# Kernel tuning notes

Hardware: AMD Instinct MI355X
Metric: run time of the kernel (lower is better)

The kernel has to match this reference:

```python
import jax, jax.numpy as jnp
import numpy as np

N_ATOMS = 100000
N_EDGES = 6400000
CUTOFF = 12.0
CUTOFF_SR = 2.0
CUTOFF_SQ = CUTOFF * CUTOFF
KEHALF = 7.199822675975274  # ASE kehalf, unit factors = 1


def poly6_switch(d, cutoff):
    # Poly6 smooth switch-off: 1 at d=0, 0 at d>=cutoff
    x = d / cutoff
    sw = 1.0 - 10.0 * x**3 + 15.0 * x**4 - 6.0 * x**5
    return jnp.where(d < cutoff, sw, jnp.zeros_like(sw))


def setup_inputs() -> dict:
    key = jax.random.key(0)
    k1, k2, k3, k4, k5 = jax.random.split(key, 5)
    atomic_charges = jax.random.normal(k1, (N_ATOMS,), dtype=jnp.float32) * 0.3
    atomic_dipoles = jax.random.normal(k2, (N_ATOMS,), dtype=jnp.float32) * 0.1
    # distances in (0.5, 13.5): some pairs inside short-range, some beyond cutoff
    distances = jax.random.uniform(k3, (N_EDGES,), dtype=jnp.float32) * 13.0 + 0.5
    idx_i = jax.random.randint(k4, (N_EDGES,), 0, N_ATOMS, dtype=jnp.int32)
    idx_j = jax.random.randint(k5, (N_EDGES,), 0, N_ATOMS, dtype=jnp.int32)
    return {
        "atomic_charges": atomic_charges,
        "atomic_dipoles": atomic_dipoles,
        "distances": distances,
        "idx_i": idx_i,
        "idx_j": idx_j,
    }


def reference(atomic_charges, atomic_dipoles, distances, idx_i, idx_j):
    # gather per-edge charges / dipoles
    qi = atomic_charges[idx_i]
    qj = atomic_charges[idx_j]
    di = atomic_dipoles[idx_i]
    dj = atomic_dipoles[idx_j]

    d = distances
    d_sh = jnp.sqrt(d * d + 1.0)  # shielded distance

    sw_off = poly6_switch(d, CUTOFF_SR)
    sw_on = 1.0 - sw_off

    # split_distance=True branch (cutoff != cutoff_short_range):
    # shifted-force Coulomb (charge-charge, ~1/d)
    E_ord_q = 1.0 / d + d / CUTOFF_SQ - 2.0 / CUTOFF
    E_sh_q = 1.0 / d_sh + d_sh / CUTOFF_SQ - 2.0 / CUTOFF
    E_q = KEHALF * qi * qj * (sw_off * E_sh_q + sw_on * E_ord_q)

    # dipole-dipole term (~1/d^3), same shielded/ordinary blending
    E_ord_d = 1.0 / d**3
    E_sh_d = 1.0 / d_sh**3
    E_d = KEHALF * di * dj * (sw_off * E_sh_d + sw_on * E_ord_d)

    E = E_q + E_d
    E = jnp.where(d <= CUTOFF, E, jnp.zeros_like(E))

    # scatter-sum per-edge energies to atoms
    return jax.ops.segment_sum(E, idx_i, num_segments=N_ATOMS)
```

## Files before the change

kernel.cpp:

```cpp
#include <hip/hip_runtime.h>
#include <hip/hip_bf16.h>
#include <hip/hip_fp16.h>

#define CUTOFF_C    12.0f
#define CUTOFF_SR_C 2.0f
#define CUTOFF_SQ_C 144.0f
#define KEHALF_C    7.199822675975274f

#define BLK1   1024

#define CH_DUO   17408
#define LUT_DUO  1024
#define CH_SOLO  33792
#define LUT_SOLO 2048

#define CH_REC   20000

__device__ __forceinline__ float edge_energy(float d, float qi, float qj,
                                             float di, float dj) {
    float inv_d   = __frcp_rn(d);
    float dsh     = __fsqrt_rn(fmaf(d, d, 1.0f));
    float inv_dsh = __frcp_rn(dsh);
    float x  = d * (1.0f / CUTOFF_SR_C);
    float x3 = x * x * x;
    float sw = fmaf(x3, fmaf(x, fmaf(x, -6.0f, 15.0f), -10.0f), 1.0f);
    float sw_off = (d < CUTOFF_SR_C) ? sw : 0.0f;
    float Eoq = inv_d   + fmaf(d,   (1.0f / CUTOFF_SQ_C), -(2.0f / CUTOFF_C));
    float Esq = inv_dsh + fmaf(dsh, (1.0f / CUTOFF_SQ_C), -(2.0f / CUTOFF_C));
    float Eq  = (KEHALF_C * qi * qj) * fmaf(sw_off, Esq - Eoq, Eoq);
    float Eod = inv_d * inv_d * inv_d;
    float Esd = inv_dsh * inv_dsh * inv_dsh;
    float Ed  = (KEHALF_C * di * dj) * fmaf(sw_off, Esd - Eod, Eod);
    return Eq + Ed;
}

__device__ __forceinline__ float2 fg_exact(float d) {
    float inv_d   = 1.0f / d;
    float dsh     = sqrtf(fmaf(d, d, 1.0f));
    float inv_dsh = 1.0f / dsh;
    float x  = d * (1.0f / CUTOFF_SR_C);
    float x3 = x * x * x;
    float sw = fmaf(x3, fmaf(x, fmaf(x, -6.0f, 15.0f), -10.0f), 1.0f);
    float sw_off = (d < CUTOFF_SR_C) ? sw : 0.0f;
    float Foq = inv_d   + fmaf(d,   (1.0f / CUTOFF_SQ_C), -(2.0f / CUTOFF_C));
    float Fsq = inv_dsh + fmaf(dsh, (1.0f / CUTOFF_SQ_C), -(2.0f / CUTOFF_C));
    float F   = fmaf(sw_off, Fsq - Foq, Foq);
    float God = inv_d * inv_d * inv_d;
    float Gsd = inv_dsh * inv_dsh * inv_dsh;
    float G   = fmaf(sw_off, Gsd - God, God);
    return make_float2(KEHALF_C * F, KEHALF_C * G);
}

__device__ __forceinline__ __half2 vw_make_exact(float d, __half2 hqdj) {
    float2 qdj = __half22float2(hqdj);
    float2 fg  = fg_exact(d);
    return __floats2half2_rn(qdj.x * fg.x, qdj.y * fg.y);
}

__device__ __forceinline__ unsigned h2bits(__half2 h) {
    union { __half2 h; unsigned u; } c; c.h = h; return c.u;
}
__device__ __forceinline__ __half2 bits2h(unsigned u) {
    union { unsigned u; __half2 h; } c; c.u = u; return c.h;
}
template <typename T>
__device__ __forceinline__ auto atom_add_h2(T* p, T v, int)
    -> decltype(atomicAdd(p, v), void()) {
    atomicAdd(p, v);
}
template <typename T>
__device__ __forceinline__ void atom_add_h2(T* p, T v, long) {
    unsigned* u = (unsigned*)p;
    unsigned old = *u, assumed;
    do {
        assumed = old;
        __half2 sum = __hadd2(bits2h(assumed), v);
        old = atomicCAS(u, assumed, h2bits(sum));
    } while (old != assumed);
}

__device__ __forceinline__ unsigned vw_bits(float d, __half2 hq) {
    float inv_d   = __builtin_amdgcn_rcpf(d);
    float dsh2    = fmaf(d, d, 1.0f);
    float inv_dsh = __builtin_amdgcn_rsqf(dsh2);
    float dsh     = dsh2 * inv_dsh;
    float x  = d * (1.0f / CUTOFF_SR_C);
    float x3 = x * x * x;
    float sw = fmaf(x3, fmaf(x, fmaf(x, -6.0f, 15.0f), -10.0f), 1.0f);
    float sw_off = (d < CUTOFF_SR_C) ? sw : 0.0f;
    float Foq = inv_d   + fmaf(d,   (1.0f / CUTOFF_SQ_C), -(2.0f / CUTOFF_C));
    float Fsq = inv_dsh + fmaf(dsh, (1.0f / CUTOFF_SQ_C), -(2.0f / CUTOFF_C));
    float F   = fmaf(sw_off, Fsq - Foq, Foq);
    float God = inv_d * inv_d * inv_d;
    float Gsd = inv_dsh * inv_dsh * inv_dsh;
    float G   = fmaf(sw_off, Gsd - God, God);
    float2 q2 = __half22float2(hq);
    __half2 vw = __floats2half2_rn((KEHALF_C * q2.x) * F, (KEHALF_C * q2.y) * G);
    return h2bits(vw);
}

__global__ __launch_bounds__(256) void pc_pack_qd_h(
    const float* __restrict__ q,
    const float* __restrict__ dip,
    __half2*     __restrict__ qd,
    int n_atoms)
{
    int a = blockIdx.x * 256 + threadIdx.x;
    if (a < n_atoms) qd[a] = __floats2half2_rn(q[a], dip[a]);
}

__global__ __launch_bounds__(256) void pc_edge_pre(
    const float*   __restrict__ dist,
    const int*     __restrict__ idx_i,
    const int*     __restrict__ idx_j,
    const __half2* __restrict__ qd,
    uint4*         __restrict__ rec4,
    int n_edges, int n4)
{
    const __half2 hzero = __floats2half2_rn(0.0f, 0.0f);
    const int t0     = blockIdx.x * 256 + (int)threadIdx.x;
    const int stride = gridDim.x * 256;
    const int4*   i4p = (const int4*)idx_i;
    const int4*   j4p = (const int4*)idx_j;
    const float4* d4p = (const float4*)dist;

    for (int g = t0; g < n4; g += stride) {
        int4   i4 = i4p[g];
        int4   j4 = j4p[g];
        float4 d4 = d4p[g];

        int   ii[4] = { i4.x, i4.y, i4.z, i4.w };
        int   jj[4] = { j4.x, j4.y, j4.z, j4.w };
        float dd[4] = { d4.x, d4.y, d4.z, d4.w };
        bool     vl[4];
        __half2  qh[4];
        unsigned ir[4], vwr[4];

        #pragma unroll
        for (int k = 0; k < 4; ++k) vl[k] = dd[k] <= CUTOFF_C;
        #pragma unroll
        for (int k = 0; k < 4; ++k) qh[k] = vl[k] ? qd[jj[k]] : hzero;
        #pragma unroll
        for (int k = 0; k < 4; ++k) {
            ir[k]  = vl[k] ? (unsigned)ii[k] : 0xFFFFFFFFu;
            vwr[k] = vw_bits(dd[k], qh[k]);
        }
        rec4[g]      = make_uint4(ir[0], vwr[0], ir[1], vwr[1]);
        rec4[n4 + g] = make_uint4(ir[2], vwr[2], ir[3], vwr[3]);
    }

    uint2* rec2 = (uint2*)rec4;
    for (int e = (n4 << 2) + t0; e < n_edges; e += stride) {
        float d = dist[e];
        bool  v = d <= CUTOFF_C;
        __half2 hq = v ? qd[idx_j[e]] : hzero;
        rec2[e] = make_uint2(v ? (unsigned)idx_i[e] : 0xFFFFFFFFu, vw_bits(d, hq));
    }
}

template <int CH, int BLK>
__global__ __launch_bounds__(BLK) void pc_scatter_rec(
    const uint4* __restrict__ rec4,
    __half2*     __restrict__ partial,
    int n_edges, int nv2, int S, int gps, int n_atoms)
{
    extern __shared__ char smem[];
    __half2* acc2 = (__half2*)smem;

    const int s = blockIdx.x % S;
    const int c = blockIdx.x / S;
    const unsigned base = (unsigned)(c * CH);
    const int lim = min(CH, n_atoms - (int)base);

    const __half2 hzero = __floats2half2_rn(0.0f, 0.0f);
    for (int i = threadIdx.x; i < CH; i += BLK) acc2[i] = hzero;
    __syncthreads();

    const int g0 = s * gps;
    const int g1 = min(g0 + gps, nv2);
    for (int g = g0 + (int)threadIdx.x; g < g1; g += BLK) {
        uint4 r = rec4[g];
        unsigned lc0 = r.x - base;
        unsigned lc1 = r.z - base;
        if (lc0 < (unsigned)CH) atom_add_h2(&acc2[lc0], bits2h(r.y), 0);
        if (lc1 < (unsigned)CH) atom_add_h2(&acc2[lc1], bits2h(r.w), 0);
    }

    if (s == S - 1 && (n_edges & 1)) {
        if (threadIdx.x == 0) {
            const uint2* rec2 = (const uint2*)rec4;
            uint2 r = rec2[n_edges - 1];
            unsigned lc = r.x - base;
            if (lc < (unsigned)CH) atom_add_h2(&acc2[lc], bits2h(r.y), 0);
        }
    }

    __syncthreads();
    __half2* row = partial + (size_t)s * n_atoms + (int)base;
    for (int i = threadIdx.x; i < lim; i += BLK) row[i] = acc2[i];
}

template <int CH, int LUTN, int BLK>
__global__ __launch_bounds__(BLK) void pc_scatter_lut(
    const float*   __restrict__ dist,
    const int*     __restrict__ idx_i,
    const int*     __restrict__ idx_j,
    const __half2* __restrict__ qd,
    __half2*       __restrict__ partial,
    int n_edges, int n4, int S, int gps, int n_atoms, int nch)
{
    extern __shared__ char smem[];
    __half2* acc2 = (__half2*)smem;
    float2*  lut  = (float2*)(smem + (size_t)CH * sizeof(__half2));

    const int s    = blockIdx.x % S;
    const int c    = blockIdx.x / S;
    const int base = c * CH;
    const int lim  = min(CH, n_atoms - base);

    const __half2 hzero = __floats2half2_rn(0.0f, 0.0f);
    for (int i = threadIdx.x; i < CH; i += BLK) acc2[i] = hzero;

    const float hstep = CUTOFF_C / (float)LUTN;
    for (int k = threadIdx.x; k <= LUTN; k += BLK) {
        float d = fmaxf((float)k * hstep, 0.25f * hstep);
        lut[k] = fg_exact(d);
    }
    __syncthreads();

    const int g0 = s * gps;
    const int g1 = min(g0 + gps, n4);
    const int4*   idxi4 = (const int4*)idx_i;
    const int4*   idxj4 = (const int4*)idx_j;
    const float4* dist4 = (const float4*)dist;
    const float   dscale = (float)LUTN / CUTOFF_C;

    for (int g = g0 + (int)threadIdx.x; g < g1; g += BLK) {
        int4   i4 = idxi4[g];
        int4   j4 = idxj4[g];
        float4 d4 = dist4[g];

        int      ii[4] = { i4.x, i4.y, i4.z, i4.w };
        int      jj[4] = { j4.x, j4.y, j4.z, j4.w };
        float    dd[4] = { d4.x, d4.y, d4.z, d4.w };
        unsigned lc[4];
        bool     vl[4];
        __half2  qh[4];

        #pragma unroll
        for (int k = 0; k < 4; ++k) {
            lc[k] = (unsigned)(ii[k] - base);
            vl[k] = (lc[k] < (unsigned)CH) && (dd[k] <= CUTOFF_C);
        }
        #pragma unroll
        for (int k = 0; k < 4; ++k)
            qh[k] = vl[k] ? qd[jj[k]] : hzero;

        #pragma unroll
        for (int k = 0; k < 4; ++k) {
            if (vl[k]) {
                float t  = dd[k] * dscale;
                int   kk = min((int)t, LUTN - 1);
                float fr = t - (float)kk;
                float2 l0 = lut[kk];
                float2 l1 = lut[kk + 1];
                float F = fmaf(fr, l1.x - l0.x, l0.x);
                float G = fmaf(fr, l1.y - l0.y, l0.y);
                float2 qdj = __half22float2(qh[k]);
                __half2 vw = __floats2half2_rn(qdj.x * F, qdj.y * G);
                atom_add_h2(&acc2[lc[k]], vw, 0);
            }
        }
    }

    if (s == S - 1) {
        for (int e = (n4 << 2) + (int)threadIdx.x; e < n_edges; e += BLK) {
            int i = idx_i[e];
            float d = dist[e];
            unsigned local = (unsigned)(i - base);
            if (local < (unsigned)CH && d <= CUTOFF_C) {
                __half2 vw = vw_make_exact(d, qd[idx_j[e]]);
                atom_add_h2(&acc2[local], vw, 0);
            }
        }
    }

    __syncthreads();
    __half2* row = partial + (size_t)s * n_atoms + base;
    for (int i = threadIdx.x; i < lim; i += BLK) row[i] = acc2[i];
}

__global__ __launch_bounds__(256) void pc_reduce_vw(
    const __half2* __restrict__ partial,
    const float*   __restrict__ q,
    const float*   __restrict__ dip,
    float*         __restrict__ out,
    int n_atoms, int S)
{
    __shared__ float2 sh[256];
    int a0   = blockIdx.x * 64;
    int lane = threadIdx.x & 63;
    int w    = threadIdx.x >> 6;
    int a    = a0 + lane;

    float sv = 0.0f, sw = 0.0f;
    if (a < n_atoms) {
        int per = S >> 2;
        const __half2* p = partial + a;
        int s = w * per, send = s + per;
        for (; s < send; ++s) {
            float2 t = __half22float2(p[(size_t)s * n_atoms]);
            sv += t.x; sw += t.y;
        }
    }
    sh[threadIdx.x] = make_float2(sv, sw);
    __syncthreads();
    if (w == 0 && a < n_atoms) {
        float2 t0 = sh[lane],       t1 = sh[64 + lane];
        float2 t2 = sh[128 + lane], t3 = sh[192 + lane];
        float fv = (t0.x + t1.x) + (t2.x + t3.x);
        float fw = (t0.y + t1.y) + (t2.y + t3.y);
        out[a] = fmaf(q[a], fv, dip[a] * fw);
    }
}

__global__ __launch_bounds__(256) void pc_dipole_edges_atomic(
    const float* __restrict__ q,
    const float* __restrict__ dip,
    const float* __restrict__ dist,
    const int*   __restrict__ idx_i,
    const int*   __restrict__ idx_j,
    float*       __restrict__ out,
    int n_edges)
{
    int t = blockIdx.x * blockDim.x + threadIdx.x;
    const int stride = gridDim.x * blockDim.x;
    for (int e = t; e < n_edges; e += stride) {
        float d = dist[e];
        if (d > CUTOFF_C) continue;
        int i = idx_i[e], j = idx_j[e];
        atomicAdd(&out[i], edge_energy(d, q[i], q[j], dip[i], dip[j]));
    }
}

static int probe_blocks(const void* f, int blk, size_t lds) {
    hipError_t e1 = hipFuncSetAttribute(
        f, hipFuncAttributeMaxDynamicSharedMemorySize, (int)lds);
    int nb = 0;
    hipError_t e2 = hipOccupancyMaxActiveBlocksPerMultiprocessor(&nb, f, blk, lds);
    if (e1 != hipSuccess || e2 != hipSuccess) return 0;
    return nb;
}

extern "C" void kernel_launch(void* const* d_in, const int* in_sizes, int n_in,
                              void* d_out, int out_size, void* d_ws, size_t ws_size,
                              hipStream_t stream) {
    const float* q     = (const float*)d_in[0];
    const float* dip   = (const float*)d_in[1];
    const float* dist  = (const float*)d_in[2];
    const int*   idx_i = (const int*)d_in[3];
    const int*   idx_j = (const int*)d_in[4];
    float*       out   = (float*)d_out;

    int n_edges = in_sizes[2];
    int n_atoms = out_size;
    int n4      = n_edges >> 2;
    int nv2     = n_edges >> 1;

    size_t qd_b   = ((size_t)n_atoms * sizeof(__half2) + 255) & ~(size_t)255;
    size_t rec_b  = (((size_t)n_edges * 8) + 255) & ~(size_t)255;
    size_t lds_rec = (size_t)CH_REC * sizeof(__half2);

    int nb_rec = probe_blocks((const void*)&pc_scatter_rec<CH_REC, BLK1>,
                              BLK1, lds_rec);

    int S_new = 0, nch_new = 0;
    if (nb_rec >= 2 && n_atoms > 0 && ws_size > qd_b + rec_b) {
        nch_new = (n_atoms + CH_REC - 1) / CH_REC;
        int cap = 512;
        S_new = (cap / nch_new) & ~7;
        size_t avail = ws_size - qd_b - rec_b;
        int S_fit = (int)(avail / ((size_t)n_atoms * sizeof(__half2))) & ~7;
        if (S_fit < S_new) S_new = S_fit;
    }

    if (S_new >= 8) {
        __half2* qd      = (__half2*)d_ws;
        uint4*   rec4    = (uint4*)((char*)d_ws + qd_b);
        __half2* partial = (__half2*)((char*)d_ws + qd_b + rec_b);
        int      gps     = (nv2 + S_new - 1) / S_new;

        pc_pack_qd_h<<<(n_atoms + 255) / 256, 256, 0, stream>>>(q, dip, qd,
                                                                n_atoms);
        int gridA = (n_edges + 1023) / 1024;
        if (gridA > 2048) gridA = 2048;
        if (gridA < 1)    gridA = 1;
        pc_edge_pre<<<gridA, 256, 0, stream>>>(dist, idx_i, idx_j, qd, rec4,
                                               n_edges, n4);
        pc_scatter_rec<CH_REC, BLK1>
            <<<S_new * nch_new, BLK1, lds_rec, stream>>>(
                rec4, partial, n_edges, nv2, S_new, gps, n_atoms);
        pc_reduce_vw<<<(n_atoms + 63) / 64, 256, 0, stream>>>(
            partial, q, dip, out, n_atoms, S_new);
        return;
    }

    size_t lds_duo  = (size_t)CH_DUO  * sizeof(__half2)
                    + (size_t)(LUT_DUO  + 1) * sizeof(float2);
    size_t lds_solo = (size_t)CH_SOLO * sizeof(__half2)
                    + (size_t)(LUT_SOLO + 1) * sizeof(float2);

    int nb_duo = probe_blocks((const void*)&pc_scatter_lut<CH_DUO, LUT_DUO, BLK1>,
                              BLK1, lds_duo);
    int nb_solo = probe_blocks((const void*)&pc_scatter_lut<CH_SOLO, LUT_SOLO, BLK1>,
                               BLK1, lds_solo);

    bool use_duo = (nb_duo >= 2);
    int  CH, nch, S, cap;
    size_t lds;
    if (use_duo) {
        CH  = CH_DUO;  lds = lds_duo;
        nch = (n_atoms + CH - 1) / CH;
        cap = 512;
    } else {
        CH  = CH_SOLO; lds = lds_solo;
        nch = (n_atoms + CH - 1) / CH;
        cap = 256;
    }
    S = (cap / nch) & ~7;
    if (S < 8) S = 8;

    size_t avail = (ws_size > qd_b) ? ws_size - qd_b : 0;
    int S_fit = (int)(avail / ((size_t)n_atoms * sizeof(__half2)));
    if (S_fit < S) S = S_fit & ~7;

    bool ok = (use_duo || nb_solo >= 1) && S >= 8 && n_atoms > 0;

    if (ok) {
        __half2* qd      = (__half2*)d_ws;
        __half2* partial = (__half2*)((char*)d_ws + qd_b);
        int      gps     = (n4 + S - 1) / S;

        pc_pack_qd_h<<<(n_atoms + 255) / 256, 256, 0, stream>>>(q, dip, qd,
                                                                n_atoms);
        if (use_duo)
            pc_scatter_lut<CH_DUO, LUT_DUO, BLK1>
                <<<S * nch, BLK1, lds, stream>>>(
                    dist, idx_i, idx_j, qd, partial, n_edges, n4, S, gps,
                    n_atoms, nch);
        else
            pc_scatter_lut<CH_SOLO, LUT_SOLO, BLK1>
                <<<S * nch, BLK1, lds, stream>>>(
                    dist, idx_i, idx_j, qd, partial, n_edges, n4, S, gps,
                    n_atoms, nch);
        pc_reduce_vw<<<(n_atoms + 63) / 64, 256, 0, stream>>>(
            partial, q, dip, out, n_atoms, S);
    } else {
        hipMemsetAsync(out, 0, (size_t)n_atoms * sizeof(float), stream);
        int grid = (n_edges + 255) / 256;
        pc_dipole_edges_atomic<<<grid, 256, 0, stream>>>(
            q, dip, dist, idx_i, idx_j, out, n_edges);
    }
}
```

Baseline: 164.5 us.

## Drop packed index records; scatter reads idx_i directly alongside per-edge values

The edge pre-pass no longer writes an 8-byte (idx_i, value) record per edge. It writes only the 4-byte half2 energy value, zeroed for edges beyond the cutoff, and no longer reads idx_i at all. The scatter kernel now reads idx_i and the value array in int4/uint4 chunks of four edges. This cuts the pre-pass's write and read traffic. The cost is that out-of-cutoff edges now perform zero-valued LDS atomics instead of being skipped. The pre-pass also switches from a capped grid-stride loop to one thread per eight edges.

```diff
diff --git a/kernel.cpp b/kernel.cpp
--- a/kernel.cpp
+++ b/kernel.cpp
@@ -109,60 +109,69 @@
     if (a < n_atoms) qd[a] = __floats2half2_rn(q[a], dip[a]);
 }
 
-__global__ __launch_bounds__(256) void pc_edge_pre(
+__global__ __launch_bounds__(256) void pc_edge_vw(
     const float*   __restrict__ dist,
-    const int*     __restrict__ idx_i,
     const int*     __restrict__ idx_j,
     const __half2* __restrict__ qd,
-    uint4*         __restrict__ rec4,
-    int n_edges, int n4)
-{
-    const __half2 hzero = __floats2half2_rn(0.0f, 0.0f);
-    const int t0     = blockIdx.x * 256 + (int)threadIdx.x;
-    const int stride = gridDim.x * 256;
-    const int4*   i4p = (const int4*)idx_i;
+    uint4*         __restrict__ vwo,
+    unsigned*      __restrict__ vws,
+    int n_edges, int n4, int half)
+{
+    const int t = blockIdx.x * 256 + (int)threadIdx.x;
     const int4*   j4p = (const int4*)idx_j;
     const float4* d4p = (const float4*)dist;
 
-    for (int g = t0; g < n4; g += stride) {
-        int4   i4 = i4p[g];
-        int4   j4 = j4p[g];
-        float4 d4 = d4p[g];
-
-        int   ii[4] = { i4.x, i4.y, i4.z, i4.w };
-        int   jj[4] = { j4.x, j4.y, j4.z, j4.w };
-        float dd[4] = { d4.x, d4.y, d4.z, d4.w };
-        bool     vl[4];
-        __half2  qh[4];
-        unsigned ir[4], vwr[4];
-
-        #pragma unroll
-        for (int k = 0; k < 4; ++k) vl[k] = dd[k] <= CUTOFF_C;
-        #pragma unroll
-        for (int k = 0; k < 4; ++k) qh[k] = vl[k] ? qd[jj[k]] : hzero;
-        #pragma unroll
-        for (int k = 0; k < 4; ++k) {
-            ir[k]  = vl[k] ? (unsigned)ii[k] : 0xFFFFFFFFu;
-            vwr[k] = vw_bits(dd[k], qh[k]);
-        }
-        rec4[g]      = make_uint4(ir[0], vwr[0], ir[1], vwr[1]);
-        rec4[n4 + g] = make_uint4(ir[2], vwr[2], ir[3], vwr[3]);
-    }
-
-    uint2* rec2 = (uint2*)rec4;
-    for (int e = (n4 << 2) + t0; e < n_edges; e += stride) {
+    if (t < half) {
+        const int  ga = t;
+        const int  gb = t + half;
+        const bool vb = gb < n4;
+        const int  gbs = vb ? gb : ga;
+
+        int4   ja = j4p[ga];
+        int4   jb = j4p[gbs];
+        float4 da = d4p[ga];
+        float4 db = d4p[gbs];
+
+        __half2 q0 = qd[ja.x], q1 = qd[ja.y], q2 = qd[ja.z], q3 = qd[ja.w];
+        __half2 q4 = qd[jb.x], q5 = qd[jb.y], q6 = qd[jb.z], q7 = qd[jb.w];
+
+        unsigned w0 = vw_bits(da.x, q0);
+        unsigned w1 = vw_bits(da.y, q1);
+        unsigned w2 = vw_bits(da.z, q2);
+        unsigned w3 = vw_bits(da.w, q3);
+        unsigned w4 = vw_bits(db.x, q4);
+        unsigned w5 = vw_bits(db.y, q5);
+        unsigned w6 = vw_bits(db.z, q6);
+        unsigned w7 = vw_bits(db.w, q7);
+
+        w0 = (da.x <= CUTOFF_C) ? w0 : 0u;
+        w1 = (da.y <= CUTOFF_C) ? w1 : 0u;
+        w2 = (da.z <= CUTOFF_C) ? w2 : 0u;
+        w3 = (da.w <= CUTOFF_C) ? w3 : 0u;
+        w4 = (db.x <= CUTOFF_C) ? w4 : 0u;
+        w5 = (db.y <= CUTOFF_C) ? w5 : 0u;
+        w6 = (db.z <= CUTOFF_C) ? w6 : 0u;
+        w7 = (db.w <= CUTOFF_C) ? w7 : 0u;
+
+        vwo[ga] = make_uint4(w0, w1, w2, w3);
+        if (vb) vwo[gb] = make_uint4(w4, w5, w6, w7);
+    }
+
+    const int tl = n_edges & 3;
+    if (blockIdx.x == 0 && (int)threadIdx.x < tl) {
+        int e = (n4 << 2) + (int)threadIdx.x;
         float d = dist[e];
-        bool  v = d <= CUTOFF_C;
-        __half2 hq = v ? qd[idx_j[e]] : hzero;
-        rec2[e] = make_uint2(v ? (unsigned)idx_i[e] : 0xFFFFFFFFu, vw_bits(d, hq));
+        unsigned w = vw_bits(d, qd[idx_j[e]]);
+        vws[e] = (d <= CUTOFF_C) ? w : 0u;
     }
 }
 
 template <int CH, int BLK>
-__global__ __launch_bounds__(BLK) void pc_scatter_rec(
-    const uint4* __restrict__ rec4,
-    __half2*     __restrict__ partial,
-    int n_edges, int nv2, int S, int gps, int n_atoms)
+__global__ __launch_bounds__(BLK) void pc_scatter_vw(
+    const int*      __restrict__ idx_i,
+    const unsigned* __restrict__ vw,
+    __half2*        __restrict__ partial,
+    int n_edges, int n4, int S, int gps, int n_atoms)
 {
     extern __shared__ char smem[];
     __half2* acc2 = (__half2*)smem;
@@ -176,22 +185,27 @@
     for (int i = threadIdx.x; i < CH; i += BLK) acc2[i] = hzero;
     __syncthreads();
 
+    const int4*  i4p = (const int4*)idx_i;
+    const uint4* v4p = (const uint4*)vw;
     const int g0 = s * gps;
-    const int g1 = min(g0 + gps, nv2);
+    const int g1 = min(g0 + gps, n4);
     for (int g = g0 + (int)threadIdx.x; g < g1; g += BLK) {
-        uint4 r = rec4[g];
-        unsigned lc0 = r.x - base;
-        unsigned lc1 = r.z - base;
-        if (lc0 < (unsigned)CH) atom_add_h2(&acc2[lc0], bits2h(r.y), 0);
-        if (lc1 < (unsigned)CH) atom_add_h2(&acc2[lc1], bits2h(r.w), 0);
-    }
-
-    if (s == S - 1 && (n_edges & 1)) {
-        if (threadIdx.x == 0) {
-            const uint2* rec2 = (const uint2*)rec4;
-            uint2 r = rec2[n_edges - 1];
-            unsigned lc = r.x - base;
-            if (lc < (unsigned)CH) atom_add_h2(&acc2[lc], bits2h(r.y), 0);
+        int4  i4 = i4p[g];
+        uint4 v4 = v4p[g];
+        unsigned lc0 = (unsigned)i4.x - base;
+        unsigned lc1 = (unsigned)i4.y - base;
+        unsigned lc2 = (unsigned)i4.z - base;
+        unsigned lc3 = (unsigned)i4.w - base;
+        if (lc0 < (unsigned)CH) atom_add_h2(&acc2[lc0], bits2h(v4.x), 0);
+        if (lc1 < (unsigned)CH) atom_add_h2(&acc2[lc1], bits2h(v4.y), 0);
+        if (lc2 < (unsigned)CH) atom_add_h2(&acc2[lc2], bits2h(v4.z), 0);
+        if (lc3 < (unsigned)CH) atom_add_h2(&acc2[lc3], bits2h(v4.w), 0);
+    }
+
+    if (s == S - 1) {
+        for (int e = (n4 << 2) + (int)threadIdx.x; e < n_edges; e += BLK) {
+            unsigned lc = (unsigned)idx_i[e] - base;
+            if (lc < (unsigned)CH) atom_add_h2(&acc2[lc], bits2h(vw[e]), 0);
         }
     }
 
@@ -365,41 +379,41 @@
     int n_edges = in_sizes[2];
     int n_atoms = out_size;
     int n4      = n_edges >> 2;
-    int nv2     = n_edges >> 1;
-
-    size_t qd_b   = ((size_t)n_atoms * sizeof(__half2) + 255) & ~(size_t)255;
-    size_t rec_b  = (((size_t)n_edges * 8) + 255) & ~(size_t)255;
+
+    size_t qd_b    = ((size_t)n_atoms * sizeof(__half2) + 255) & ~(size_t)255;
+    size_t vw_b    = (((size_t)n_edges * 4) + 255) & ~(size_t)255;
     size_t lds_rec = (size_t)CH_REC * sizeof(__half2);
 
-    int nb_rec = probe_blocks((const void*)&pc_scatter_rec<CH_REC, BLK1>,
+    int nb_rec = probe_blocks((const void*)&pc_scatter_vw<CH_REC, BLK1>,
                               BLK1, lds_rec);
 
     int S_new = 0, nch_new = 0;
-    if (nb_rec >= 2 && n_atoms > 0 && ws_size > qd_b + rec_b) {
+    if (nb_rec >= 2 && n_atoms > 0 && n4 > 0 && ws_size > qd_b + vw_b) {
         nch_new = (n_atoms + CH_REC - 1) / CH_REC;
         int cap = 512;
         S_new = (cap / nch_new) & ~7;
-        size_t avail = ws_size - qd_b - rec_b;
+        size_t avail = ws_size - qd_b - vw_b;
         int S_fit = (int)(avail / ((size_t)n_atoms * sizeof(__half2))) & ~7;
         if (S_fit < S_new) S_new = S_fit;
     }
 
     if (S_new >= 8) {
-        __half2* qd      = (__half2*)d_ws;
-        uint4*   rec4    = (uint4*)((char*)d_ws + qd_b);
-        __half2* partial = (__half2*)((char*)d_ws + qd_b + rec_b);
-        int      gps     = (nv2 + S_new - 1) / S_new;
+        __half2*  qd      = (__half2*)d_ws;
+        unsigned* vw      = (unsigned*)((char*)d_ws + qd_b);
+        __half2*  partial = (__half2*)((char*)d_ws + qd_b + vw_b);
+        int       gps     = (n4 + S_new - 1) / S_new;
+        int       half    = (n4 + 1) >> 1;
+        int       gridA   = (half + 255) / 256;
+        if (gridA < 1) gridA = 1;
 
         pc_pack_qd_h<<<(n_atoms + 255) / 256, 256, 0, stream>>>(q, dip, qd,
                                                                 n_atoms);
-        int gridA = (n_edges + 1023) / 1024;
-        if (gridA > 2048) gridA = 2048;
-        if (gridA < 1)    gridA = 1;
-        pc_edge_pre<<<gridA, 256, 0, stream>>>(dist, idx_i, idx_j, qd, rec4,
-                                               n_edges, n4);
-        pc_scatter_rec<CH_REC, BLK1>
+        pc_edge_vw<<<gridA, 256, 0, stream>>>(dist, idx_j, qd,
+                                              (uint4*)vw, vw,
+                                              n_edges, n4, half);
+        pc_scatter_vw<CH_REC, BLK1>
             <<<S_new * nch_new, BLK1, lds_rec, stream>>>(
-                rec4, partial, n_edges, nv2, S_new, gps, n_atoms);
+                idx_i, vw, partial, n_edges, n4, S_new, gps, n_atoms);
         pc_reduce_vw<<<(n_atoms + 63) / 64, 256, 0, stream>>>(
             partial, q, dip, out, n_atoms, S_new);
         return;
```

Result: no change. 162.2 us (-1.4%).
